# Performance work log

Hardware: AMD Instinct MI355X
Metric: run time of the kernel (lower is better)

## Reference

```python
import jax, jax.numpy as jnp
import numpy as np

B, S, H = 32, 2048, 1024

def setup_inputs() -> dict:
    key = jax.random.key(0)
    ks = jax.random.split(key, 8)
    s = 1.0 / np.sqrt(H)
    return {
        "query": jax.random.normal(ks[0], (B, 1, H), jnp.float32),
        "keys": jax.random.normal(ks[1], (B, S, H), jnp.float32),
        "Wa_w": jax.random.normal(ks[2], (H, H), jnp.float32) * s,
        "Wa_b": jax.random.normal(ks[3], (H,), jnp.float32) * s,
        "Ua_w": jax.random.normal(ks[4], (H, H), jnp.float32) * s,
        "Ua_b": jax.random.normal(ks[5], (H,), jnp.float32) * s,
        "Va_w": jax.random.normal(ks[6], (1, H), jnp.float32) * s,
        "Va_b": jax.random.normal(ks[7], (1,), jnp.float32) * s,
    }

def reference(query, keys, Wa_w, Wa_b, Ua_w, Ua_b, Va_w, Va_b):
    # Wa(query): (B,1,H); Ua(keys): (B,S,H); broadcast add -> (B,S,H)
    q = jnp.einsum('bqh,oh->bqo', query, Wa_w) + Wa_b
    k = jnp.einsum('bsh,oh->bso', keys, Ua_w) + Ua_b
    h = jnp.tanh(q + k)                              # (B,S,H)
    scores = jnp.einsum('bsh,oh->bso', h, Va_w) + Va_b  # (B,S,1)
    scores = scores[:, :, 0][:, None, :]             # (B,1,S)
    weights = jax.nn.softmax(scores, axis=-1)        # (B,1,S)
    context = jnp.einsum('bqs,bsh->bqh', weights, keys)  # (B,1,H)
    return context, weights
```

## Files before the change

### kernel.cpp

```cpp
#include <hip/hip_runtime.h>
#include <hip/hip_bf16.h>

#define HDIM 1024
#define SEQ  2048
#define BATCH 32
#define M_TOTAL (BATCH * SEQ)
#define BM 256
#define BN 256
#define BK 32
#define KSTEPS (HDIM / BK)
#define NSLICE 16

typedef __bf16 bf16x8 __attribute__((ext_vector_type(8)));
typedef float  f32x4  __attribute__((ext_vector_type(4)));
typedef unsigned short u16;
#define AS1 __attribute__((address_space(1)))
#define AS3 __attribute__((address_space(3)))

__device__ __forceinline__ u16 f2bf(float f) {
    unsigned int u = __float_as_uint(f);
    u += 0x7FFFu + ((u >> 16) & 1u);
    return (u16)(u >> 16);
}

__global__ __launch_bounds__(256) void cvt_kernel(const float* __restrict__ in,
                                                  u16* __restrict__ out) {
    size_t i = ((size_t)blockIdx.x * 256 + threadIdx.x) * 8;
    float4 f0 = *(const float4*)(in + i);
    float4 f1 = *(const float4*)(in + i + 4);
    uint4 v;
    v.x = (unsigned)f2bf(f0.x) | ((unsigned)f2bf(f0.y) << 16);
    v.y = (unsigned)f2bf(f0.z) | ((unsigned)f2bf(f0.w) << 16);
    v.z = (unsigned)f2bf(f1.x) | ((unsigned)f2bf(f1.y) << 16);
    v.w = (unsigned)f2bf(f1.z) | ((unsigned)f2bf(f1.w) << 16);
    *(uint4*)(out + i) = v;
}

__global__ __launch_bounds__(256) void qb_kernel(const float* __restrict__ query,
                                                 const float* __restrict__ Wa_w,
                                                 const float* __restrict__ Wa_b,
                                                 const float* __restrict__ Ua_b,
                                                 float* __restrict__ qb) {
    __shared__ float qs[HDIM];
    const int b = blockIdx.x;
    const int tid = threadIdx.x;
    ((float4*)qs)[tid] = ((const float4*)(query + b * HDIM))[tid];
    __syncthreads();
    const int lane = tid & 63;
    const int w = tid >> 6;
    const int obase = blockIdx.y * 64 + w * 16;
    for (int i = 0; i < 16; i++) {
        int o = obase + i;
        const float4* wrow = (const float4*)(Wa_w + (size_t)o * HDIM);
        float s = 0.f;
        #pragma unroll
        for (int j = 0; j < 4; j++) {
            float4 wv = wrow[j * 64 + lane];
            float4 qv = ((const float4*)qs)[j * 64 + lane];
            s += wv.x * qv.x + wv.y * qv.y + wv.z * qv.z + wv.w * qv.w;
        }
        #pragma unroll
        for (int m = 1; m < 64; m <<= 1) s += __shfl_xor(s, m);
        if (lane == 0) qb[b * HDIM + o] = s + Wa_b[o] + Ua_b[o];
    }
}

__global__ __launch_bounds__(512, 2) void gemm_score_kernel(const u16* __restrict__ keysb,
                                                            const u16* __restrict__ uab,
                                                            const float* __restrict__ qb,
                                                            const float* __restrict__ vaw,
                                                            float* __restrict__ sp) {
    __shared__ __align__(16) u16 As[4][BM * BK];
    __shared__ __align__(16) u16 Bs[4][BN * BK];

    const int tid  = threadIdx.x;
    const int lane = tid & 63;
    const int w    = tid >> 6;
    const int wm   = w >> 2;
    const int wn   = w & 3;

    const int bid = blockIdx.y * 4 + blockIdx.x;
    const int swz = (bid & 7) * 128 + (bid >> 3);
    const int bx  = swz & 3;
    const int by  = swz >> 2;
    const int n0  = bx * BN;
    const int m0  = by * BM;

    const int srow = lane >> 2;
    const int cs   = (lane & 3) ^ ((lane >> 3) & 3);
    const u16* gA0 = keysb + (size_t)(m0 + w * 32 + srow) * HDIM + cs * 8;
    const u16* gB0 = uab   + (size_t)(n0 + w * 32 + srow) * HDIM + cs * 8;
    const int ldst = w * 32 * BK;

    const int fr = lane & 15;
    const int fq = lane >> 4;
    const int sA = fq ^ ((fr >> 1) & 3);
    const int aoff = (wm * 128 + fr) * BK + sA * 8;
    const int boff = (wn * 64  + fr) * BK + sA * 8;

    f32x4 acc[8][4] = {};

#define STAGE_A(kt) { \
    u16* d = &As[(kt) & 3][ldst]; \
    __builtin_amdgcn_global_load_lds((AS1 void*)(gA0 + (size_t)(kt) * BK), (AS3 void*)d, 16, 0, 0); \
    __builtin_amdgcn_global_load_lds((AS1 void*)(gA0 + (size_t)(kt) * BK + 16 * HDIM), (AS3 void*)(d + 16 * BK), 16, 0, 0); }
#define STAGE_B(kt) { \
    u16* d = &Bs[(kt) & 3][ldst]; \
    __builtin_amdgcn_global_load_lds((AS1 void*)(gB0 + (size_t)(kt) * BK), (AS3 void*)d, 16, 0, 0); \
    __builtin_amdgcn_global_load_lds((AS1 void*)(gB0 + (size_t)(kt) * BK + 16 * HDIM), (AS3 void*)(d + 16 * BK), 16, 0, 0); }

    STAGE_A(0) STAGE_B(0)
    STAGE_A(1) STAGE_B(1)
    STAGE_A(2) STAGE_B(2)

    for (int t = 0; t < KSTEPS; ++t) {
        if (t < KSTEPS - 2)       asm volatile("s_waitcnt vmcnt(8)" ::: "memory");
        else if (t == KSTEPS - 2) asm volatile("s_waitcnt vmcnt(4)" ::: "memory");
        else                      asm volatile("s_waitcnt vmcnt(0)" ::: "memory");
        __builtin_amdgcn_s_barrier();

        const u16* ap = &As[t & 3][aoff];
        const u16* bp = &Bs[t & 3][boff];
        bf16x8 a[8], b[4];

        #pragma unroll
        for (int i = 0; i < 4; i++) a[i] = *(const bf16x8*)(ap + i * 16 * BK);
        #pragma unroll
        for (int i = 0; i < 4; i++) b[i] = *(const bf16x8*)(bp + i * 16 * BK);
        if (t + 3 < KSTEPS) STAGE_A(t + 3)
        __builtin_amdgcn_s_barrier();
        asm volatile("s_waitcnt lgkmcnt(0)" ::: "memory");
        __builtin_amdgcn_sched_barrier(0);
        __builtin_amdgcn_s_setprio(1);
        #pragma unroll
        for (int mi = 0; mi < 4; mi++)
            #pragma unroll
            for (int ni = 0; ni < 4; ni++)
                acc[mi][ni] = __builtin_amdgcn_mfma_f32_16x16x32_bf16(a[mi], b[ni], acc[mi][ni], 0, 0, 0);
        __builtin_amdgcn_s_setprio(0);
        __builtin_amdgcn_s_barrier();

        #pragma unroll
        for (int i = 4; i < 8; i++) a[i] = *(const bf16x8*)(ap + i * 16 * BK);
        if (t + 3 < KSTEPS) STAGE_B(t + 3)
        __builtin_amdgcn_s_barrier();
        asm volatile("s_waitcnt lgkmcnt(0)" ::: "memory");
        __builtin_amdgcn_sched_barrier(0);
        __builtin_amdgcn_s_setprio(1);
        #pragma unroll
        for (int mi = 4; mi < 8; mi++)
            #pragma unroll
            for (int ni = 0; ni < 4; ni++)
                acc[mi][ni] = __builtin_amdgcn_mfma_f32_16x16x32_bf16(a[mi], b[ni], acc[mi][ni], 0, 0, 0);
        __builtin_amdgcn_s_setprio(0);
    }
#undef STAGE_A
#undef STAGE_B

    const int bidx = m0 >> 11;
    float qv[4], vv[4];
    #pragma unroll
    for (int ni = 0; ni < 4; ni++) {
        int n_g = n0 + wn * 64 + ni * 16 + fr;
        qv[ni] = qb[bidx * HDIM + n_g];
        vv[ni] = vaw[n_g];
    }
    const int slice = bx * 4 + wn;
    float* sl = sp + ((size_t)slice * BATCH + bidx) * SEQ;
    #pragma unroll
    for (int mi = 0; mi < 8; mi++) {
        #pragma unroll
        for (int r = 0; r < 4; r++) {
            float p = 0.f;
            #pragma unroll
            for (int ni = 0; ni < 4; ni++) {
                float x = acc[mi][ni][r] + qv[ni];
                float e = __expf(2.f * x);
                p += (1.f - 2.f / (e + 1.f)) * vv[ni];
            }
            p += __shfl_xor(p, 1);
            p += __shfl_xor(p, 2);
            p += __shfl_xor(p, 4);
            p += __shfl_xor(p, 8);
            if (fr == 0) {
                int s_g = (m0 + wm * 128 + mi * 16 + fq * 4 + r) & (SEQ - 1);
                sl[s_g] = p;
            }
        }
    }
}

__global__ __launch_bounds__(256) void softmax_kernel(const float* __restrict__ sp,
                                                      float* __restrict__ weights,
                                                      float* __restrict__ ctx) {
    __shared__ float red[4];
    const int b = blockIdx.x;
    const int tid = threadIdx.x;
    float4 z = {0.f, 0.f, 0.f, 0.f};
    ((float4*)(ctx + b * HDIM))[tid] = z;
    float v[8];
    float mx = -1e30f;
    #pragma unroll
    for (int i = 0; i < 8; i++) {
        int s = tid + i * 256;
        float a = 0.f;
        #pragma unroll
        for (int j = 0; j < NSLICE; j++) a += sp[((size_t)j * BATCH + b) * SEQ + s];
        v[i] = a;
        mx = fmaxf(mx, a);
    }
    #pragma unroll
    for (int m = 1; m < 64; m <<= 1) mx = fmaxf(mx, __shfl_xor(mx, m));
    if ((tid & 63) == 0) red[tid >> 6] = mx;
    __syncthreads();
    mx = fmaxf(fmaxf(red[0], red[1]), fmaxf(red[2], red[3]));
    float sum = 0.f;
    #pragma unroll
    for (int i = 0; i < 8; i++) { v[i] = __expf(v[i] - mx); sum += v[i]; }
    #pragma unroll
    for (int m = 1; m < 64; m <<= 1) sum += __shfl_xor(sum, m);
    __syncthreads();
    if ((tid & 63) == 0) red[tid >> 6] = sum;
    __syncthreads();
    sum = red[0] + red[1] + red[2] + red[3];
    float inv = 1.f / sum;
    #pragma unroll
    for (int i = 0; i < 8; i++) weights[b * SEQ + tid + i * 256] = v[i] * inv;
}

__global__ __launch_bounds__(256) void context_kernel(const u16* __restrict__ keysb,
                                                      const float* __restrict__ weights,
                                                      float* __restrict__ ctx) {
    __shared__ float wsm[256];
    const int b = blockIdx.x;
    const int s0 = blockIdx.y * 256;
    const int tid = threadIdx.x;
    wsm[tid] = weights[b * SEQ + s0 + tid];
    __syncthreads();
    const int hq = tid & 127;
    const int sh = (tid >> 7) * 128;
    float a0 = 0.f, a1 = 0.f, a2 = 0.f, a3 = 0.f;
    float a4 = 0.f, a5 = 0.f, a6 = 0.f, a7 = 0.f;
    const uint4* kp = (const uint4*)(keysb + (size_t)b * SEQ * HDIM
                                     + (size_t)(s0 + sh) * HDIM) + hq;
    #pragma unroll 8
    for (int s = 0; s < 128; s++) {
        uint4 kv = kp[s * 128];
        float wv = wsm[sh + s];
        a0 += wv * __uint_as_float(kv.x << 16);
        a1 += wv * __uint_as_float(kv.x & 0xFFFF0000u);
        a2 += wv * __uint_as_float(kv.y << 16);
        a3 += wv * __uint_as_float(kv.y & 0xFFFF0000u);
        a4 += wv * __uint_as_float(kv.z << 16);
        a5 += wv * __uint_as_float(kv.z & 0xFFFF0000u);
        a6 += wv * __uint_as_float(kv.w << 16);
        a7 += wv * __uint_as_float(kv.w & 0xFFFF0000u);
    }
    float* o = ctx + b * HDIM + hq * 8;
    atomicAdd(o + 0, a0);
    atomicAdd(o + 1, a1);
    atomicAdd(o + 2, a2);
    atomicAdd(o + 3, a3);
    atomicAdd(o + 4, a4);
    atomicAdd(o + 5, a5);
    atomicAdd(o + 6, a6);
    atomicAdd(o + 7, a7);
}

extern "C" void kernel_launch(void* const* d_in, const int* in_sizes, int n_in,
                              void* d_out, int out_size, void* d_ws, size_t ws_size,
                              hipStream_t stream) {
    const float* query = (const float*)d_in[0];
    const float* keys  = (const float*)d_in[1];
    const float* Wa_w  = (const float*)d_in[2];
    const float* Wa_b  = (const float*)d_in[3];
    const float* Ua_w  = (const float*)d_in[4];
    const float* Ua_b  = (const float*)d_in[5];
    const float* Va_w  = (const float*)d_in[6];
    float* out = (float*)d_out;

    char* ws = (char*)d_ws;
    u16*  keysb = (u16*)ws;
    u16*  uab   = (u16*)(ws + 134217728);
    float* qb   = (float*)(ws + 134217728 + 2097152);
    float* sp   = (float*)(ws + 134217728 + 2097152 + 131072);

    cvt_kernel<<<(BATCH * SEQ * HDIM) / 2048, 256, 0, stream>>>(keys, keysb);
    cvt_kernel<<<(HDIM * HDIM) / 2048, 256, 0, stream>>>(Ua_w, uab);
    qb_kernel<<<dim3(BATCH, HDIM / 64), 256, 0, stream>>>(query, Wa_w, Wa_b, Ua_b, qb);
    gemm_score_kernel<<<dim3(HDIM / BN, M_TOTAL / BM), 512, 0, stream>>>(keysb, uab, qb, Va_w, sp);
    softmax_kernel<<<BATCH, 256, 0, stream>>>(sp, out + BATCH * HDIM, out);
    context_kernel<<<dim3(BATCH, 8), 256, 0, stream>>>(keysb, out + BATCH * HDIM, out);
}
```

Measured before the change: 629.8 us.

## Software-pipeline LDS fragment reads into registers and cut barriers per k-step

```diff
diff --git a/kernel.cpp b/kernel.cpp
--- a/kernel.cpp
+++ b/kernel.cpp
@@ -65,6 +65,15 @@
     }
 }
 
+#define DSREAD(dst, base, imm) \
+    asm volatile("ds_read_b128 %0, %1 offset:" #imm : "=v"(dst) : "v"(base))
+
+#define MFMA4(mi, av, b0v, b1v, b2v, b3v) \
+    acc[mi][0] = __builtin_amdgcn_mfma_f32_16x16x32_bf16(av, b0v, acc[mi][0], 0, 0, 0); \
+    acc[mi][1] = __builtin_amdgcn_mfma_f32_16x16x32_bf16(av, b1v, acc[mi][1], 0, 0, 0); \
+    acc[mi][2] = __builtin_amdgcn_mfma_f32_16x16x32_bf16(av, b2v, acc[mi][2], 0, 0, 0); \
+    acc[mi][3] = __builtin_amdgcn_mfma_f32_16x16x32_bf16(av, b3v, acc[mi][3], 0, 0, 0);
+
 __global__ __launch_bounds__(512, 2) void gemm_score_kernel(const u16* __restrict__ keysb,
                                                             const u16* __restrict__ uab,
                                                             const float* __restrict__ qb,
@@ -95,8 +104,10 @@
     const int fr = lane & 15;
     const int fq = lane >> 4;
     const int sA = fq ^ ((fr >> 1) & 3);
-    const int aoff = (wm * 128 + fr) * BK + sA * 8;
-    const int boff = (wn * 64  + fr) * BK + sA * 8;
+    const unsigned aB0 = (unsigned)(unsigned long long)(const AS3 u16*)&As[0][0]
+                       + (unsigned)(((wm * 128 + fr) * BK + sA * 8) * 2);
+    const unsigned bB0 = (unsigned)(unsigned long long)(const AS3 u16*)&Bs[0][0]
+                       + (unsigned)(((wn * 64  + fr) * BK + sA * 8) * 2);
 
     f32x4 acc[8][4] = {};
 
@@ -109,51 +120,64 @@
     __builtin_amdgcn_global_load_lds((AS1 void*)(gB0 + (size_t)(kt) * BK), (AS3 void*)d, 16, 0, 0); \
     __builtin_amdgcn_global_load_lds((AS1 void*)(gB0 + (size_t)(kt) * BK + 16 * HDIM), (AS3 void*)(d + 16 * BK), 16, 0, 0); }
 
+    bf16x8 a0, a1, a2, a3, a4, a5, a6, a7;
+    bf16x8 bA0, bA1, bA2, bA3, bB0v, bB1v, bB2v, bB3v;
+
     STAGE_A(0) STAGE_B(0)
     STAGE_A(1) STAGE_B(1)
     STAGE_A(2) STAGE_B(2)
-
-    for (int t = 0; t < KSTEPS; ++t) {
-        if (t < KSTEPS - 2)       asm volatile("s_waitcnt vmcnt(8)" ::: "memory");
-        else if (t == KSTEPS - 2) asm volatile("s_waitcnt vmcnt(4)" ::: "memory");
-        else                      asm volatile("s_waitcnt vmcnt(0)" ::: "memory");
-        __builtin_amdgcn_s_barrier();
-
-        const u16* ap = &As[t & 3][aoff];
-        const u16* bp = &Bs[t & 3][boff];
-        bf16x8 a[8], b[4];
-
-        #pragma unroll
-        for (int i = 0; i < 4; i++) a[i] = *(const bf16x8*)(ap + i * 16 * BK);
-        #pragma unroll
-        for (int i = 0; i < 4; i++) b[i] = *(const bf16x8*)(bp + i * 16 * BK);
-        if (t + 3 < KSTEPS) STAGE_A(t + 3)
-        __builtin_amdgcn_s_barrier();
-        asm volatile("s_waitcnt lgkmcnt(0)" ::: "memory");
-        __builtin_amdgcn_sched_barrier(0);
-        __builtin_amdgcn_s_setprio(1);
-        #pragma unroll
-        for (int mi = 0; mi < 4; mi++)
-            #pragma unroll
-            for (int ni = 0; ni < 4; ni++)
-                acc[mi][ni] = __builtin_amdgcn_mfma_f32_16x16x32_bf16(a[mi], b[ni], acc[mi][ni], 0, 0, 0);
-        __builtin_amdgcn_s_setprio(0);
-        __builtin_amdgcn_s_barrier();
-
-        #pragma unroll
-        for (int i = 4; i < 8; i++) a[i] = *(const bf16x8*)(ap + i * 16 * BK);
-        if (t + 3 < KSTEPS) STAGE_B(t + 3)
-        __builtin_amdgcn_s_barrier();
-        asm volatile("s_waitcnt lgkmcnt(0)" ::: "memory");
-        __builtin_amdgcn_sched_barrier(0);
-        __builtin_amdgcn_s_setprio(1);
-        #pragma unroll
-        for (int mi = 4; mi < 8; mi++)
-            #pragma unroll
-            for (int ni = 0; ni < 4; ni++)
-                acc[mi][ni] = __builtin_amdgcn_mfma_f32_16x16x32_bf16(a[mi], b[ni], acc[mi][ni], 0, 0, 0);
-        __builtin_amdgcn_s_setprio(0);
-    }
+    asm volatile("s_waitcnt vmcnt(4)" ::: "memory");
+    __builtin_amdgcn_s_barrier();
+    DSREAD(a0, aB0, 0);    DSREAD(a1, aB0, 1024);
+    DSREAD(a2, aB0, 2048); DSREAD(a3, aB0, 3072);
+    DSREAD(bA0, bB0, 0);    DSREAD(bA1, bB0, 1024);
+    DSREAD(bA2, bB0, 2048); DSREAD(bA3, bB0, 3072);
+
+#define TILE(t, bc0, bc1, bc2, bc3, bn0, bn1, bn2, bn3) { \
+    const unsigned at = aB0 + (((t) & 3) << 14);              \
+     \
+    if ((t) + 3 < KSTEPS) STAGE_A((t) + 3) \
+    DSREAD(a4, at, 4096); DSREAD(a5, at, 5120); \
+    DSREAD(a6, at, 6144); DSREAD(a7, at, 7168); \
+    asm volatile("s_waitcnt lgkmcnt(4)" ::: "memory");        \
+    __builtin_amdgcn_sched_barrier(0); \
+    __builtin_amdgcn_s_setprio(1); \
+    MFMA4(0, a0, bc0, bc1, bc2, bc3) \
+    MFMA4(1, a1, bc0, bc1, bc2, bc3) \
+    MFMA4(2, a2, bc0, bc1, bc2, bc3) \
+    MFMA4(3, a3, bc0, bc1, bc2, bc3) \
+    __builtin_amdgcn_s_setprio(0); \
+     \
+    if ((t) + 3 < KSTEPS) STAGE_B((t) + 3) \
+    if ((t) + 1 < KSTEPS) { \
+        const unsigned an = aB0 + ((((t) + 1) & 3) << 14); \
+        const unsigned bn = bB0 + ((((t) + 1) & 3) << 14); \
+        DSREAD(a0, an, 0);    DSREAD(a1, an, 1024); \
+        DSREAD(a2, an, 2048); DSREAD(a3, an, 3072); \
+        DSREAD(bn0, bn, 0);    DSREAD(bn1, bn, 1024); \
+        DSREAD(bn2, bn, 2048); DSREAD(bn3, bn, 3072); \
+        asm volatile("s_waitcnt lgkmcnt(8)" ::: "memory");    \
+    } else { \
+        asm volatile("s_waitcnt lgkmcnt(0)" ::: "memory"); \
+    } \
+    __builtin_amdgcn_sched_barrier(0); \
+    __builtin_amdgcn_s_setprio(1); \
+    MFMA4(4, a4, bc0, bc1, bc2, bc3) \
+    MFMA4(5, a5, bc0, bc1, bc2, bc3) \
+    MFMA4(6, a6, bc0, bc1, bc2, bc3) \
+    MFMA4(7, a7, bc0, bc1, bc2, bc3) \
+    __builtin_amdgcn_s_setprio(0); \
+     \
+    if ((t) + 1 < KSTEPS - 2) asm volatile("s_waitcnt vmcnt(4)" ::: "memory"); \
+    else                      asm volatile("s_waitcnt vmcnt(0)" ::: "memory"); \
+    __builtin_amdgcn_s_barrier(); \
+}
+
+    for (int t = 0; t < KSTEPS; t += 2) {
+        TILE(t,     bA0, bA1, bA2, bA3, bB0v, bB1v, bB2v, bB3v)
+        TILE(t + 1, bB0v, bB1v, bB2v, bB3v, bA0, bA1, bA2, bA3)
+    }
+#undef TILE
 #undef STAGE_A
 #undef STAGE_B
 
```

Measured after the change: 598.6 us. 1.05x faster.
